# Kernel tuning notes

Hardware: AMD Instinct MI355X
Metric: run time of the kernel (lower is better)

Reference implementation:

```python
import jax, jax.numpy as jnp
import numpy as np

BOX = 120          # box_size
RES = 1.0          # resolution (also Gaussian sigma)
NTYPES = 11        # num_atom_types (hard-coded in module)
D = 2              # splat half-width in cells -> (2D+1)^3 = 125 voxels/atom
B = 4
NATOMS = 2200      # 200 atoms per type


def setup_inputs() -> dict:
    key = jax.random.key(0)
    # atoms uniformly inside the box interior so splats mostly land in-bounds
    coords = jax.random.uniform(key, (B, NATOMS * 3), dtype=jnp.float32,
                                minval=20.0, maxval=100.0)
    per_type = NATOMS // NTYPES
    num_atoms_of_type = jnp.full((B, NTYPES), per_type, dtype=jnp.int32)
    offsets = jnp.tile(jnp.arange(NTYPES, dtype=jnp.int32) * per_type, (B, 1))
    return {"input_coords": coords,
            "num_atoms_of_type": num_atoms_of_type,
            "offsets": offsets}


def _splat(coords, num_atoms_of_type, offsets):
    # coords: [B, N, 3]; per-atom Gaussian splat into typed volume
    Bn, N, _ = coords.shape
    atom_idx = jnp.arange(N)

    def per_batch_types(off, num):
        # atoms [off[t], off[t]+num[t]) belong to type t
        t = jnp.clip(jnp.searchsorted(off, atom_idx, side='right') - 1, 0, NTYPES - 1)
        valid = (atom_idx >= off[t]) & (atom_idx < off[t] + num[t])
        return t, valid

    types, valid = jax.vmap(per_batch_types)(offsets, num_atoms_of_type)  # [B,N]

    # (2D+1)^3 window of integer cell offsets
    w = jnp.arange(-D, D + 1)
    wx, wy, wz = jnp.meshgrid(w, w, w, indexing='ij')
    win = jnp.stack([wx.ravel(), wy.ravel(), wz.ravel()], axis=-1)  # [W,3]

    base = jnp.floor(coords / RES).astype(jnp.int32)                 # [B,N,3]
    cells = base[:, :, None, :] + win[None, None, :, :]              # [B,N,W,3]
    centers = cells.astype(coords.dtype) * RES                       # voxel coords
    r2 = jnp.sum((centers - coords[:, :, None, :]) ** 2, axis=-1)    # [B,N,W]
    vals = jnp.exp(-r2 / (RES * RES))                                # Gaussian density

    inb = jnp.all((cells >= 0) & (cells < BOX), axis=-1)             # [B,N,W]
    ok = inb & valid[:, :, None]
    flat = (types[:, :, None] * (BOX * BOX * BOX)
            + cells[..., 0] * (BOX * BOX) + cells[..., 1] * BOX + cells[..., 2])
    flat = jnp.where(ok, flat, NTYPES * BOX * BOX * BOX)  # out-of-range -> dropped
    vals = jnp.where(ok, vals, jnp.zeros_like(vals))

    def scatter(f, v):
        vol = jnp.zeros((NTYPES * BOX * BOX * BOX,), dtype=coords.dtype)
        return vol.at[f.ravel()].add(v.ravel(), mode='drop')

    vol = jax.vmap(scatter)(flat, vals)
    return vol.reshape(Bn, NTYPES, BOX, BOX, BOX)


def reference(input_coords, num_atoms_of_type, offsets):
    coords = input_coords.reshape(input_coords.shape[0], -1, 3)
    return _splat(coords, num_atoms_of_type, offsets)
```

## Files before the change

kernel.cpp:

```cpp
#include <hip/hip_runtime.h>


#define BOX    120
#define NTYPES 11
#define DHALF  2
#define BOX3   (BOX * BOX * BOX)

#define BINSZ  4
#define NBIN   30
#define NBIN2  (NBIN * NBIN)
#define CAP    64

#define YT     4
#define NYT    (BOX / YT)
#define SCAP   128
#define TILEF  (NTYPES * YT * BOX)

typedef float v4f __attribute__((ext_vector_type(4)));

__global__ void bin_kernel(const float* __restrict__ coords,
                           const int*  __restrict__ num_atoms_of_type,
                           const int*  __restrict__ offsets,
                           float4* __restrict__ bins,
                           int*    __restrict__ counts,
                           int batch, int natoms) {
    int gid = blockIdx.x * blockDim.x + threadIdx.x;
    if (gid >= batch * natoms) return;
    int b = gid / natoms;
    int i = gid - b * natoms;

    const float* c = coords + ((long long)b * natoms + i) * 3;
    float x = c[0], y = c[1], z = c[2];

    const int* off = offsets           + b * NTYPES;
    const int* num = num_atoms_of_type + b * NTYPES;

    int t = 0;
#pragma unroll
    for (int k = 1; k < NTYPES; ++k)
        if (off[k] <= i) t = k;
    if (!(i >= off[t] && i < off[t] + num[t])) return;

    int bx = (int)floorf(x);
    int by = (int)floorf(y);
    int bz = (int)floorf(z);
    if (bx < -DHALF || bx >= BOX + DHALF ||
        by < -DHALF || by >= BOX + DHALF ||
        bz < -DHALF || bz >= BOX + DHALF) return;

    int cbx = min(BOX - 1, max(0, bx)) / BINSZ;
    int cby = min(BOX - 1, max(0, by)) / BINSZ;
    int bin = b * NBIN2 + cbx * NBIN + cby;

    int slot = atomicAdd(&counts[bin], 1);
    if (slot < CAP)
        bins[(long long)bin * CAP + slot] =
            make_float4(x, y, z, __int_as_float(t));
}

__global__ __launch_bounds__(256)
void gather_kernel(const float4* __restrict__ bins,
                   const int*    __restrict__ counts,
                   float* __restrict__ out) {
    int bid = blockIdx.x;
    int yt = bid % NYT; bid /= NYT;
    int x  = bid % BOX; bid /= BOX;
    int b  = bid;
    int y0 = yt * YT;
    float xf = (float)x;

    __shared__ __align__(16) float tile[TILEF];
    __shared__ float4 srt[SCAP];
    __shared__ int cnt;

    float4* t4 = reinterpret_cast<float4*>(tile);
    for (int i = threadIdx.x; i < TILEF / 4; i += 256)
        t4[i] = make_float4(0.f, 0.f, 0.f, 0.f);
    if (threadIdx.x == 0) cnt = 0;
    __syncthreads();

    int bxlo = max(0, x - DHALF) / BINSZ;
    int bxhi = min(BOX - 1, x + DHALF) / BINSZ;
    int bylo = max(0, y0 - DHALF) / BINSZ;
    int byhi = min(BOX - 1, y0 + YT - 1 + DHALF) / BINSZ;

    for (int cbx = bxlo; cbx <= bxhi; ++cbx) {
        for (int cby = bylo; cby <= byhi; ++cby) {
            int bin = b * NBIN2 + cbx * NBIN + cby;
            int c = min(counts[bin], CAP);
            const float4* lst = bins + (long long)bin * CAP;
            for (int j = threadIdx.x; j < c; j += 256) {
                float4 a = lst[j];
                float abx = floorf(a.x);
                float aby = floorf(a.y);
                if (fabsf(xf - abx) <= (float)DHALF &&
                    aby >= (float)(y0 - DHALF) &&
                    aby <= (float)(y0 + YT - 1 + DHALF)) {
                    int slot = atomicAdd(&cnt, 1);
                    if (slot < SCAP) {
                        float dx = xf - a.x;
                        srt[slot] = make_float4(a.y, a.z, dx * dx, a.w);
                    }
                }
            }
        }
    }
    __syncthreads();
    int n = min(cnt, SCAP);

    for (int w = threadIdx.x; w < n * 25; w += 256) {
        int j   = w / 25;
        int rem = w - j * 25;
        int iy  = rem / 5;
        int iz  = rem - iy * 5;
        float4 a = srt[j];
        float ay = a.x, az = a.y, dx2 = a.z;
        int t   = __float_as_int(a.w);
        int aby = (int)floorf(ay);
        int abz = (int)floorf(az);
        int cy  = aby + iy - DHALF;
        int cz  = abz + iz - DHALF;
        if (cy < y0 || cy >= y0 + YT || (unsigned)cz >= (unsigned)BOX) continue;
        float dy = (float)cy - ay;
        float dz = (float)cz - az;
        float r2 = fmaf(dy, dy, fmaf(dz, dz, dx2));
        float v  = __expf(-r2);
        atomicAdd(&tile[(t * YT + (cy - y0)) * BOX + cz], v);
    }
    __syncthreads();

    long long obase = (long long)b * NTYPES * BOX3
                    + (long long)x * (BOX * BOX) + (long long)y0 * BOX;
    const v4f* t4v = reinterpret_cast<const v4f*>(tile);
    const int C4 = YT * BOX / 4;
    for (int i = threadIdx.x; i < NTYPES * C4; i += 256) {
        int k = i / C4;
        int r = i - k * C4;
        v4f v = t4v[k * C4 + r];
        __builtin_nontemporal_store(
            v, reinterpret_cast<v4f*>(&out[obase + (long long)k * BOX3 + r * 4]));
    }
}

extern "C" void kernel_launch(void* const* d_in, const int* in_sizes, int n_in,
                              void* d_out, int out_size, void* d_ws, size_t ws_size,
                              hipStream_t stream) {
    const float* coords = (const float*)d_in[0];
    const int*   num    = (const int*)d_in[1];
    const int*   off    = (const int*)d_in[2];
    float*       out    = (float*)d_out;

    int batch  = in_sizes[1] / NTYPES;
    int natoms = in_sizes[0] / (3 * batch);

    int    nbins  = batch * NBIN2;
    int*   counts = (int*)d_ws;
    size_t bins_off = ((size_t)nbins * sizeof(int) + 15) & ~(size_t)15;
    float4* bins  = (float4*)((char*)d_ws + bins_off);

    hipMemsetAsync(counts, 0, (size_t)nbins * sizeof(int), stream);

    int natom_threads = batch * natoms;
    bin_kernel<<<(natom_threads + 255) / 256, 256, 0, stream>>>(
        coords, num, off, bins, counts, batch, natoms);

    gather_kernel<<<batch * BOX * NYT, 256, 0, stream>>>(bins, counts, out);
}
```

Measured before the change: 310.7 us.

## Fuse binning into gather kernel by scanning all atoms per block

```diff
diff --git a/kernel.cpp b/kernel.cpp
--- a/kernel.cpp
+++ b/kernel.cpp
@@ -6,11 +6,6 @@
 #define DHALF  2
 #define BOX3   (BOX * BOX * BOX)
 
-#define BINSZ  4
-#define NBIN   30
-#define NBIN2  (NBIN * NBIN)
-#define CAP    64
-
 #define YT     4
 #define NYT    (BOX / YT)
 #define SCAP   128
@@ -18,50 +13,12 @@
 
 typedef float v4f __attribute__((ext_vector_type(4)));
 
-__global__ void bin_kernel(const float* __restrict__ coords,
-                           const int*  __restrict__ num_atoms_of_type,
-                           const int*  __restrict__ offsets,
-                           float4* __restrict__ bins,
-                           int*    __restrict__ counts,
-                           int batch, int natoms) {
-    int gid = blockIdx.x * blockDim.x + threadIdx.x;
-    if (gid >= batch * natoms) return;
-    int b = gid / natoms;
-    int i = gid - b * natoms;
-
-    const float* c = coords + ((long long)b * natoms + i) * 3;
-    float x = c[0], y = c[1], z = c[2];
-
-    const int* off = offsets           + b * NTYPES;
-    const int* num = num_atoms_of_type + b * NTYPES;
-
-    int t = 0;
-#pragma unroll
-    for (int k = 1; k < NTYPES; ++k)
-        if (off[k] <= i) t = k;
-    if (!(i >= off[t] && i < off[t] + num[t])) return;
-
-    int bx = (int)floorf(x);
-    int by = (int)floorf(y);
-    int bz = (int)floorf(z);
-    if (bx < -DHALF || bx >= BOX + DHALF ||
-        by < -DHALF || by >= BOX + DHALF ||
-        bz < -DHALF || bz >= BOX + DHALF) return;
-
-    int cbx = min(BOX - 1, max(0, bx)) / BINSZ;
-    int cby = min(BOX - 1, max(0, by)) / BINSZ;
-    int bin = b * NBIN2 + cbx * NBIN + cby;
-
-    int slot = atomicAdd(&counts[bin], 1);
-    if (slot < CAP)
-        bins[(long long)bin * CAP + slot] =
-            make_float4(x, y, z, __int_as_float(t));
-}
-
 __global__ __launch_bounds__(256)
-void gather_kernel(const float4* __restrict__ bins,
-                   const int*    __restrict__ counts,
-                   float* __restrict__ out) {
+void fused_kernel(const float* __restrict__ coords,
+                  const int*  __restrict__ num_atoms_of_type,
+                  const int*  __restrict__ offsets,
+                  float* __restrict__ out,
+                  int natoms) {
     int bid = blockIdx.x;
     int yt = bid % NYT; bid /= NYT;
     int x  = bid % BOX; bid /= BOX;
@@ -79,30 +36,30 @@
     if (threadIdx.x == 0) cnt = 0;
     __syncthreads();
 
-    int bxlo = max(0, x - DHALF) / BINSZ;
-    int bxhi = min(BOX - 1, x + DHALF) / BINSZ;
-    int bylo = max(0, y0 - DHALF) / BINSZ;
-    int byhi = min(BOX - 1, y0 + YT - 1 + DHALF) / BINSZ;
+    const int* off = offsets           + b * NTYPES;
+    const int* num = num_atoms_of_type + b * NTYPES;
+    const float* cbase = coords + (long long)b * natoms * 3;
 
-    for (int cbx = bxlo; cbx <= bxhi; ++cbx) {
-        for (int cby = bylo; cby <= byhi; ++cby) {
-            int bin = b * NBIN2 + cbx * NBIN + cby;
-            int c = min(counts[bin], CAP);
-            const float4* lst = bins + (long long)bin * CAP;
-            for (int j = threadIdx.x; j < c; j += 256) {
-                float4 a = lst[j];
-                float abx = floorf(a.x);
-                float aby = floorf(a.y);
-                if (fabsf(xf - abx) <= (float)DHALF &&
-                    aby >= (float)(y0 - DHALF) &&
-                    aby <= (float)(y0 + YT - 1 + DHALF)) {
-                    int slot = atomicAdd(&cnt, 1);
-                    if (slot < SCAP) {
-                        float dx = xf - a.x;
-                        srt[slot] = make_float4(a.y, a.z, dx * dx, a.w);
-                    }
-                }
-            }
+    float ylo = (float)(y0 - DHALF);
+    float yhi = (float)(y0 + YT - 1 + DHALF);
+    for (int j = threadIdx.x; j < natoms; j += 256) {
+        float ax = cbase[j * 3 + 0];
+        float ay = cbase[j * 3 + 1];
+        float az = cbase[j * 3 + 2];
+        float abx = floorf(ax);
+        float aby = floorf(ay);
+        if (fabsf(xf - abx) > (float)DHALF) continue;
+        if (aby < ylo || aby > yhi) continue;
+        int t = 0;
+#pragma unroll
+        for (int k = 1; k < NTYPES; ++k)
+            if (off[k] <= j) t = k;
+        if (!(j >= off[t] && j < off[t] + num[t])) continue;
+
+        int slot = atomicAdd(&cnt, 1);
+        if (slot < SCAP) {
+            float dx = xf - ax;
+            srt[slot] = make_float4(ay, az, dx * dx, __int_as_float(t));
         }
     }
     __syncthreads();
@@ -153,16 +110,6 @@
     int batch  = in_sizes[1] / NTYPES;
     int natoms = in_sizes[0] / (3 * batch);
 
-    int    nbins  = batch * NBIN2;
-    int*   counts = (int*)d_ws;
-    size_t bins_off = ((size_t)nbins * sizeof(int) + 15) & ~(size_t)15;
-    float4* bins  = (float4*)((char*)d_ws + bins_off);
-
-    hipMemsetAsync(counts, 0, (size_t)nbins * sizeof(int), stream);
-
-    int natom_threads = batch * natoms;
-    bin_kernel<<<(natom_threads + 255) / 256, 256, 0, stream>>>(
-        coords, num, off, bins, counts, batch, natoms);
-
-    gather_kernel<<<batch * BOX * NYT, 256, 0, stream>>>(bins, counts, out);
+    fused_kernel<<<batch * BOX * NYT, 256, 0, stream>>>(
+        coords, num, off, out, natoms);
 }
```

Result: no change. 316.9 us (+2.0%).
